# Kernel optimization log

Measured on AMD Instinct MI355X. Metric: run time of the kernel, lower is better.

Reference implementation:

```python
import jax, jax.numpy as jnp
import numpy as np
import math

HORIZONS = (1, 5, 21)
TEMP = 0.07
N_NEG = 128
B, T, D = 16, 512, 256


def _normalize(x):
    # F.normalize(dim=-1): x / max(||x||, eps)
    return x / jnp.maximum(jnp.linalg.norm(x, axis=-1, keepdims=True), 1e-12)


def setup_inputs() -> dict:
    key = jax.random.key(0)
    k1, k2, k3 = jax.random.split(key, 3)
    z_seq = jax.random.normal(k1, (B, T, D), dtype=jnp.float32)
    # stacked per-horizon Linear weights (nn.Linear applies x @ W.T)
    preds = jax.random.normal(k2, (len(HORIZONS), D, D), dtype=jnp.float32) / np.float32(np.sqrt(D))
    neg_idx = jax.random.randint(k3, (len(HORIZONS), B * T, N_NEG), 0, B * T, dtype=jnp.int64)
    return {"z_seq": z_seq, "preds": preds, "neg_idx": neg_idx}


def reference(z_seq, preds, neg_idx):
    raw_w = {k: 1.0 / math.sqrt(k) for k in HORIZONS}
    tot_w = sum(raw_w.values())
    # detached, normalized pool of all timesteps used as negatives
    all_z = jax.lax.stop_gradient(_normalize(z_seq.reshape(B * T, D)))
    total = jnp.float32(0.0)
    for i, k in enumerate(HORIZONS):
        if k >= T:
            continue
        L = T - k
        # predictor: Linear without bias -> anchor @ W.T
        z_pred = jnp.einsum('bld,ed->ble', z_seq[:, :L, :], preds[i]).reshape(B * L, D)
        z_pred = _normalize(z_pred)
        z_pos = jax.lax.stop_gradient(_normalize(z_seq[:, k:, :].reshape(B * L, D)))
        idx = neg_idx[i, :B * L]                    # [B*L, N_NEG]
        z_neg = all_z[idx]                          # [B*L, N_NEG, D]
        pos_logit = jnp.sum(z_pred * z_pos, axis=-1, keepdims=True) / TEMP   # [B*L, 1]
        neg_logits = jnp.einsum('nkd,nd->nk', z_neg, z_pred) / TEMP          # [B*L, N_NEG]
        logits = jnp.concatenate([pos_logit, neg_logits], axis=1)
        # cross-entropy with label 0
        loss = jnp.mean(jax.nn.logsumexp(logits, axis=1) - logits[:, 0])
        total = total + jnp.float32(raw_w[k] / tot_w) * loss
    return total
```

## Files before the change

kernel.cpp:

```cpp
#include <hip/hip_runtime.h>
#include <math.h>

constexpr int Bc = 16, Tc = 512, Dc = 256, NNEGc = 128, BTc = Bc * Tc;
constexpr float TEMP_INV = 1.0f / 0.07f;
constexpr float SCALE4 = 21.875f;
constexpr float QSCALE4 = TEMP_INV / (SCALE4 * SCALE4);
constexpr float FMAXL = TEMP_INV;
constexpr int GX = 2043;
constexpr int NPART = 3 * GX;

typedef __attribute__((ext_vector_type(8))) short short8;
typedef __attribute__((ext_vector_type(4))) float f32x4;
typedef __attribute__((ext_vector_type(4))) _Float16 f16x4;
typedef __attribute__((ext_vector_type(2))) _Float16 h2;

struct HP { int L, N, kh; float scale; long long nxOff; };
struct HP3 { HP h[3]; };

__device__ inline unsigned packh2(float a, float b) {
    h2 p = {(_Float16)a, (_Float16)b};
    return __builtin_bit_cast(unsigned, p);
}
__device__ inline float dot2(unsigned a, unsigned b, float c) {
#if __has_builtin(__builtin_amdgcn_fdot2)
    return __builtin_amdgcn_fdot2(__builtin_bit_cast(h2, a), __builtin_bit_cast(h2, b), c, false);
#else
    h2 x = __builtin_bit_cast(h2, a), y = __builtin_bit_cast(h2, b);
    return c + (float)x.x * (float)y.x + (float)x.y * (float)y.y;
#endif
}
__device__ inline int sdot8(unsigned a, unsigned b, int c) {
#if __has_builtin(__builtin_amdgcn_sdot8)
    return __builtin_amdgcn_sdot8((int)a, (int)b, c, false);
#else
#pragma unroll
    for (int i = 0; i < 8; ++i) {
        int xa = ((int)(a << (28 - 4 * i))) >> 28;
        int xb = ((int)(b << (28 - 4 * i))) >> 28;
        c += xa * xb;
    }
    return c;
#endif
}
__device__ inline unsigned q4x4(float a, float b, float c, float d) {
    int qa = (int)rintf(fminf(fmaxf(a * SCALE4, -7.0f), 7.0f));
    int qb = (int)rintf(fminf(fmaxf(b * SCALE4, -7.0f), 7.0f));
    int qc = (int)rintf(fminf(fmaxf(c * SCALE4, -7.0f), 7.0f));
    int qd = (int)rintf(fminf(fmaxf(d * SCALE4, -7.0f), 7.0f));
    return (qa & 0xF) | ((qb & 0xF) << 4) | ((qc & 0xF) << 8) | ((qd & 0xF) << 12);
}

__global__ __launch_bounds__(256) void k_norm(const float* __restrict__ z,
                                              const float* __restrict__ preds,
                                              unsigned* __restrict__ az,
                                              unsigned short* __restrict__ ani4,
                                              unsigned* __restrict__ Wh) {
    if (blockIdx.x < 96) {
        int base = blockIdx.x * 2048 + threadIdx.x * 8;
        float4 w0 = reinterpret_cast<const float4*>(preds + base)[0];
        float4 w1 = reinterpret_cast<const float4*>(preds + base)[1];
        uint4 o;
        o.x = packh2(w0.x, w0.y); o.y = packh2(w0.z, w0.w);
        o.z = packh2(w1.x, w1.y); o.w = packh2(w1.z, w1.w);
        reinterpret_cast<uint4*>(Wh)[blockIdx.x * 256 + threadIdx.x] = o;
    }
    int wid = threadIdx.x >> 6, lane = threadIdx.x & 63;
    int row = blockIdx.x * 4 + wid;
    float4 v = reinterpret_cast<const float4*>(z)[row * 64 + lane];
    float s = v.x * v.x + v.y * v.y + v.z * v.z + v.w * v.w;
#pragma unroll
    for (int off = 32; off; off >>= 1) s += __shfl_xor(s, off, 64);
    float inv = 1.0f / fmaxf(sqrtf(s), 1e-12f);
    float a = v.x * inv, b = v.y * inv, c = v.z * inv, d = v.w * inv;
    reinterpret_cast<uint2*>(az)[row * 64 + lane] = make_uint2(packh2(a, b), packh2(c, d));
    ani4[row * 64 + lane] = (unsigned short)q4x4(a, b, c, d);
}

__global__ __launch_bounds__(256) void k_gemm(const unsigned* __restrict__ az,
                                              const unsigned* __restrict__ Wh,
                                              _Float16* __restrict__ zp) {
    __shared__ uint4 As[2048];
    __shared__ uint4 Bs[2048];
    int wave = threadIdx.x >> 6, lane = threadIdx.x & 63;
    int t = threadIdx.x;
    int m0 = blockIdx.x * 64, g0 = blockIdx.y * 64;
    const uint4* A4 = reinterpret_cast<const uint4*>(az) + (size_t)m0 * 32;
    const uint4* B4 = reinterpret_cast<const uint4*>(Wh) + (size_t)g0 * 32;
#pragma unroll
    for (int i = 0; i < 8; ++i) {
        int f = i * 256 + t;
        int r = f >> 5, c = f & 31;
        int sw = r * 32 + ((c ^ r) & 31);
        As[sw] = A4[f];
        Bs[sw] = B4[f];
    }
    __syncthreads();
    int mrow = lane & 15, kq = lane >> 4;
    f32x4 acc[4] = {f32x4{0,0,0,0}, f32x4{0,0,0,0}, f32x4{0,0,0,0}, f32x4{0,0,0,0}};
    int arow = wave * 16 + mrow;
#pragma unroll
    for (int kb = 0; kb < 8; ++kb) {
        int col = kb * 4 + kq;
        uint4 ua = As[arow * 32 + ((col ^ arow) & 31)];
        short8 a = __builtin_bit_cast(short8, ua);
#pragma unroll
        for (int nt = 0; nt < 4; ++nt) {
            int brow = nt * 16 + mrow;
            uint4 ub = Bs[brow * 32 + ((col ^ brow) & 31)];
            acc[nt] = __builtin_amdgcn_mfma_f32_16x16x32_f16(
                a, __builtin_bit_cast(short8, ub), acc[nt], 0, 0, 0);
        }
    }
#pragma unroll
    for (int nt = 0; nt < 4; ++nt) {
        int g = g0 + nt * 16 + mrow;
        int h = g >> 8, e = g & 255;
        _Float16* dst = zp + ((size_t)h * BTc + m0 + wave * 16 + kq * 4) * Dc + e;
#pragma unroll
        for (int r = 0; r < 4; ++r) dst[(size_t)r * Dc] = (_Float16)acc[nt][r];
    }
}

__global__ __launch_bounds__(256, 4) void k_loss(const unsigned* __restrict__ az,
                                                 const unsigned* __restrict__ ani4,
                                                 const _Float16* __restrict__ zp_base,
                                                 const int* __restrict__ nx_base,
                                                 float* __restrict__ partials,
                                                 HP3 P) {
    HP hp = P.h[blockIdx.y];
    __shared__ uint4 zqm[4][8];
    __shared__ float partial[4];
    int wid = threadIdx.x >> 6, lane = threadIdx.x & 63;
    int g = lane >> 3, s = lane & 7;
    int n = blockIdx.x * 4 + wid;
    float contrib = 0.0f;
    if (n < hp.N) {
        const int* nx = nx_base + hp.nxOff + (size_t)n * NNEGc;
        int i1 = nx[lane], i2 = nx[lane + 64];
        int idxp[16];
#pragma unroll
        for (int p = 0; p < 16; ++p)
            idxp[p] = __shfl(p < 8 ? i1 : i2, (p & 7) * 8 + g, 64);

        const uint4* ni4 = reinterpret_cast<const uint4*>(ani4);
        uint4 buf[2];
        buf[0] = ni4[(size_t)idxp[0] * 8 + s];

        int b = n / hp.L, l = n - b * hp.L;
        int row = b * Tc + l;
        f16x4 hv = reinterpret_cast<const f16x4*>(
                       zp_base + ((size_t)blockIdx.y * BTc + row) * Dc)[lane];
        uint2 pw = reinterpret_cast<const uint2*>(az + (size_t)(row + hp.kh) * 128)[lane];
        float4 v = make_float4((float)hv.x, (float)hv.y, (float)hv.z, (float)hv.w);
        float sq = v.x * v.x + v.y * v.y + v.z * v.z + v.w * v.w;
#pragma unroll
        for (int off = 32; off; off >>= 1) sq += __shfl_xor(sq, off, 64);
        float inv = 1.0f / fmaxf(sqrtf(sq), 1e-12f);
        v.x *= inv; v.y *= inv; v.z *= inv; v.w *= inv;
        reinterpret_cast<unsigned short*>(zqm[wid])[lane] =
            (unsigned short)q4x4(v.x, v.y, v.z, v.w);
        float pd = dot2(pw.y, packh2(v.z, v.w), dot2(pw.x, packh2(v.x, v.y), 0.0f));
#pragma unroll
        for (int off = 32; off; off >>= 1) pd += __shfl_xor(pd, off, 64);
        float pos = pd * TEMP_INV;
        uint4 zs = zqm[wid][s];

        float sl = 0.0f;
#pragma unroll
        for (int p = 0; p < 16; ++p) {
            int cur = p & 1, nxt = cur ^ 1;
            if (p < 15) buf[nxt] = ni4[(size_t)idxp[p + 1] * 8 + s];
            uint4 gl = buf[cur];
            int acc = 0;
            acc = sdot8(gl.x, zs.x, acc);
            acc = sdot8(gl.y, zs.y, acc);
            acc = sdot8(gl.z, zs.z, acc);
            acc = sdot8(gl.w, zs.w, acc);
            acc += __shfl_xor(acc, 1, 64);
            acc += __shfl_xor(acc, 2, 64);
            acc += __shfl_xor(acc, 4, 64);
            sl += __expf((float)acc * QSCALE4 - FMAXL);
        }
        sl += __shfl_xor(sl, 8, 64);
        sl += __shfl_xor(sl, 16, 64);
        sl += __shfl_xor(sl, 32, 64);
        float S = sl + __expf(pos - FMAXL);
        contrib = (FMAXL + __logf(S) - pos) * hp.scale;
    }
    if (lane == 0) partial[wid] = contrib;
    __syncthreads();
    if (threadIdx.x == 0)
        partials[blockIdx.y * GX + blockIdx.x] =
            partial[0] + partial[1] + partial[2] + partial[3];
}

__global__ __launch_bounds__(256) void k_final(const float* __restrict__ partials,
                                               float* __restrict__ out) {
    __shared__ float ws[4];
    int wid = threadIdx.x >> 6, lane = threadIdx.x & 63;
    float s = 0.0f;
    for (int i = threadIdx.x; i < NPART; i += 256) s += partials[i];
#pragma unroll
    for (int off = 32; off; off >>= 1) s += __shfl_xor(s, off, 64);
    if (lane == 0) ws[wid] = s;
    __syncthreads();
    if (threadIdx.x == 0) out[0] = ws[0] + ws[1] + ws[2] + ws[3];
}

extern "C" void kernel_launch(void* const* d_in, const int* in_sizes, int n_in,
                              void* d_out, int out_size, void* d_ws, size_t ws_size,
                              hipStream_t stream) {
    const float* z     = (const float*)d_in[0];
    const float* preds = (const float*)d_in[1];
    const int*   nidx  = (const int*)d_in[2];
    float* out = (float*)d_out;

    unsigned*       az   = (unsigned*)d_ws;
    unsigned short* ani4 = (unsigned short*)((char*)d_ws + (size_t)4194304);
    unsigned*       Wh   = (unsigned*)((char*)d_ws + (size_t)5242880);
    _Float16*       zp   = (_Float16*)((char*)d_ws + (size_t)5636096);
    float*          part = (float*)((char*)d_ws + (size_t)18219008);

    const int ks[3] = {1, 5, 21};
    double rw[3] = {1.0, 1.0 / sqrt(5.0), 1.0 / sqrt(21.0)};
    double tot = rw[0] + rw[1] + rw[2];

    HP3 P;
    for (int i = 0; i < 3; ++i) {
        int L = Tc - ks[i], N = Bc * L;
        P.h[i].L = L; P.h[i].N = N; P.h[i].kh = ks[i];
        P.h[i].scale = (float)(rw[i] / tot / (double)N);
        P.h[i].nxOff = (long long)i * BTc * NNEGc;
    }

    k_norm<<<BTc / 4, 256, 0, stream>>>(z, preds, az, ani4, Wh);
    k_gemm<<<dim3(BTc / 64, (3 * Dc) / 64), 256, 0, stream>>>(az, Wh, zp);
    k_loss<<<dim3(GX, 3), 256, 0, stream>>>(az, (const unsigned*)ani4, zp, nidx, part, P);
    k_final<<<1, 256, 0, stream>>>(part, out);
}
```

Baseline: 108.8 us.

## Process two negatives per iteration and pack their dot reductions into one shuffle

```diff
diff --git a/kernel.cpp b/kernel.cpp
--- a/kernel.cpp
+++ b/kernel.cpp
@@ -137,14 +137,12 @@
     if (n < hp.N) {
         const int* nx = nx_base + hp.nxOff + (size_t)n * NNEGc;
         int i1 = nx[lane], i2 = nx[lane + 64];
-        int idxp[16];
-#pragma unroll
-        for (int p = 0; p < 16; ++p)
-            idxp[p] = __shfl(p < 8 ? i1 : i2, (p & 7) * 8 + g, 64);
-
         const uint4* ni4 = reinterpret_cast<const uint4*>(ani4);
-        uint4 buf[2];
-        buf[0] = ni4[(size_t)idxp[0] * 8 + s];
+        int ia = __shfl(i1, 0 * 8 + g, 64);
+        int ib = __shfl(i1, 1 * 8 + g, 64);
+        uint4 buf[2][2];
+        buf[0][0] = ni4[(size_t)ia * 8 + s];
+        buf[0][1] = ni4[(size_t)ib * 8 + s];
 
         int b = n / hp.L, l = n - b * hp.L;
         int row = b * Tc + l;
@@ -167,19 +165,28 @@
 
         float sl = 0.0f;
 #pragma unroll
-        for (int p = 0; p < 16; ++p) {
-            int cur = p & 1, nxt = cur ^ 1;
-            if (p < 15) buf[nxt] = ni4[(size_t)idxp[p + 1] * 8 + s];
-            uint4 gl = buf[cur];
-            int acc = 0;
-            acc = sdot8(gl.x, zs.x, acc);
-            acc = sdot8(gl.y, zs.y, acc);
-            acc = sdot8(gl.z, zs.z, acc);
-            acc = sdot8(gl.w, zs.w, acc);
-            acc += __shfl_xor(acc, 1, 64);
-            acc += __shfl_xor(acc, 2, 64);
-            acc += __shfl_xor(acc, 4, 64);
-            sl += __expf((float)acc * QSCALE4 - FMAXL);
+        for (int k = 0; k < 8; ++k) {
+            int cur = k & 1, nxt = cur ^ 1;
+            if (k < 7) {
+                int p0 = 2 * k + 2, p1 = 2 * k + 3;
+                int na = __shfl(p0 < 8 ? i1 : i2, (p0 & 7) * 8 + g, 64);
+                int nb = __shfl(p1 < 8 ? i1 : i2, (p1 & 7) * 8 + g, 64);
+                buf[nxt][0] = ni4[(size_t)na * 8 + s];
+                buf[nxt][1] = ni4[(size_t)nb * 8 + s];
+            }
+            uint4 ga = buf[cur][0], gb = buf[cur][1];
+            int aa = 0, ab = 0;
+            aa = sdot8(ga.x, zs.x, aa); aa = sdot8(ga.y, zs.y, aa);
+            aa = sdot8(ga.z, zs.z, aa); aa = sdot8(ga.w, zs.w, aa);
+            ab = sdot8(gb.x, zs.x, ab); ab = sdot8(gb.y, zs.y, ab);
+            ab = sdot8(gb.z, zs.z, ab); ab = sdot8(gb.w, zs.w, ab);
+            unsigned pk = ((unsigned)(aa + 2048) << 16) | (unsigned)(ab + 2048);
+            pk += (unsigned)__shfl_xor((int)pk, 1, 64);
+            pk += (unsigned)__shfl_xor((int)pk, 2, 64);
+            pk += (unsigned)__shfl_xor((int)pk, 4, 64);
+            float la = (float)((int)(pk >> 16) - 16384);
+            float lb = (float)((int)(pk & 0xffffu) - 16384);
+            sl += __expf(la * QSCALE4 - FMAXL) + __expf(lb * QSCALE4 - FMAXL);
         }
         sl += __shfl_xor(sl, 8, 64);
         sl += __shfl_xor(sl, 16, 64);
```

Result: faster. 105.2 us (-3.3%).
